# Optimization experiments

Measured on AMD Instinct MI355X. Metric: run time of the kernel, lower is better.

The kernel has to match this reference:

```python
import jax, jax.numpy as jnp
import numpy as np

B, S, D, E, H = 4, 2048, 1024, 8, 2048


def setup_inputs() -> dict:
    key = jax.random.key(0)
    ks = jax.random.split(key, 8)
    s_in = 1.0 / np.sqrt(D)   # torch Linear default init scale (uniform bound)
    s_hid = 1.0 / np.sqrt(H)
    return {
        "x": jax.random.normal(ks[0], (B, S, D), dtype=jnp.float32),
        "W1": jax.random.uniform(ks[1], (E, D, H), minval=-s_in, maxval=s_in, dtype=jnp.float32),
        "b1": jax.random.uniform(ks[2], (E, H), minval=-s_in, maxval=s_in, dtype=jnp.float32),
        "W2": jax.random.uniform(ks[3], (E, H, D), minval=-s_hid, maxval=s_hid, dtype=jnp.float32),
        "b2": jax.random.uniform(ks[4], (E, D), minval=-s_hid, maxval=s_hid, dtype=jnp.float32),
        "Wg": jax.random.uniform(ks[5], (D, E), minval=-s_in, maxval=s_in, dtype=jnp.float32),
        "bg": jax.random.uniform(ks[6], (E,), minval=-s_in, maxval=s_in, dtype=jnp.float32),
    }


def reference(x, W1, b1, W2, b2, Wg, bg):
    # All-experts dense MoE (eval mode: dropout is identity).
    # hidden: [B,S,E,H]
    h = jax.nn.relu(jnp.einsum("bsd,edh->bseh", x, W1) + b1)
    # expert outputs: [B,S,E,D]
    expert_out = jnp.einsum("bseh,ehd->bsed", h, W2) + b2
    # gate (raw linear, no softmax in original): [B,S,E]
    gate = jnp.einsum("bsd,de->bse", x, Wg) + bg
    # gate-weighted sum over experts -> [B,S,D]
    return jnp.einsum("bse,bsed->bsd", gate, expert_out)
```

## Files before the change

### kernel.cpp

```cpp
#include <hip/hip_runtime.h>

#define NTOK 8192
#define DDIM 1024
#define HDIM 2048
#define NEXP 8
#define GEXP 2

typedef unsigned short u16;
typedef short bf16x8 __attribute__((ext_vector_type(8)));
typedef float f32x4 __attribute__((ext_vector_type(4)));
typedef float float4_t __attribute__((ext_vector_type(4)));

__device__ __forceinline__ u16 f2bf(float f) {
  unsigned u = __float_as_uint(f);
  u += 0x7FFFu + ((u >> 16) & 1u);
  return (u16)(u >> 16);
}

#define GLOAD_LDS16(gp, lp)                                                     \
  __builtin_amdgcn_global_load_lds(                                             \
      (const __attribute__((address_space(1))) unsigned int*)(gp),              \
      (__attribute__((address_space(3))) unsigned int*)(lp), 16, 0, 0)

__global__ void k_prep(const float* __restrict__ x, const float* __restrict__ Wg,
                       const float* __restrict__ bg,
                       u16* __restrict__ xb, float* __restrict__ gate) {
  const int tok = (blockIdx.x * 256 + threadIdx.x) >> 6;
  const int lane = threadIdx.x & 63;
  const float* xr = x + (size_t)tok * DDIM;
  u16* xo = xb + (size_t)tok * DDIM;
  float s[NEXP];
#pragma unroll
  for (int e = 0; e < NEXP; ++e) s[e] = 0.f;
#pragma unroll
  for (int it = 0; it < 2; ++it) {
    const int d0 = lane * 8 + it * 512;
    float4_t v0 = *(const float4_t*)(xr + d0);
    float4_t v1 = *(const float4_t*)(xr + d0 + 4);
    union { bf16x8 v; u16 h[8]; } u;
    u.h[0] = f2bf(v0.x); u.h[1] = f2bf(v0.y); u.h[2] = f2bf(v0.z); u.h[3] = f2bf(v0.w);
    u.h[4] = f2bf(v1.x); u.h[5] = f2bf(v1.y); u.h[6] = f2bf(v1.z); u.h[7] = f2bf(v1.w);
    *(bf16x8*)(xo + d0) = u.v;
    float xv[8] = {v0.x, v0.y, v0.z, v0.w, v1.x, v1.y, v1.z, v1.w};
#pragma unroll
    for (int j = 0; j < 8; ++j) {
      const float4_t w0 = *(const float4_t*)(Wg + (size_t)(d0 + j) * NEXP);
      const float4_t w1 = *(const float4_t*)(Wg + (size_t)(d0 + j) * NEXP + 4);
      s[0] += xv[j] * w0.x; s[1] += xv[j] * w0.y;
      s[2] += xv[j] * w0.z; s[3] += xv[j] * w0.w;
      s[4] += xv[j] * w1.x; s[5] += xv[j] * w1.y;
      s[6] += xv[j] * w1.z; s[7] += xv[j] * w1.w;
    }
  }
#pragma unroll
  for (int off = 32; off; off >>= 1)
#pragma unroll
    for (int e = 0; e < NEXP; ++e) s[e] += __shfl_down(s[e], off);
  if (lane == 0) {
#pragma unroll
    for (int e = 0; e < NEXP; ++e) gate[(size_t)tok * NEXP + e] = s[e] + bg[e];
  }
}

__global__ void k_transpose(const float* __restrict__ in, u16* __restrict__ out,
                            int R, int C, size_t oexp, int orstride) {
  __shared__ float t[64][65];
  const int rb = blockIdx.x * 64, cb = blockIdx.y * 64;
  const float* pin = in + (size_t)blockIdx.z * R * C;
  u16* pout = out + (size_t)blockIdx.z * oexp;
  const int tid = threadIdx.x;
  {
    const int r = tid >> 4;
    const int c4 = (tid & 15) * 4;
#pragma unroll
    for (int i = 0; i < 4; ++i) {
      float4_t v = *(const float4_t*)(pin + (size_t)(rb + r + 16 * i) * C + cb + c4);
      t[r + 16 * i][c4 + 0] = v.x;
      t[r + 16 * i][c4 + 1] = v.y;
      t[r + 16 * i][c4 + 2] = v.z;
      t[r + 16 * i][c4 + 3] = v.w;
    }
  }
  __syncthreads();
  {
    const int oc = tid >> 3;
    const int r8 = (tid & 7) * 8;
#pragma unroll
    for (int jp = 0; jp < 2; ++jp) {
      const int ocol = oc + 32 * jp;
      union { bf16x8 v; u16 h[8]; } u;
#pragma unroll
      for (int k = 0; k < 8; ++k) u.h[k] = f2bf(t[r8 + k][ocol]);
      *(bf16x8*)(pout + (size_t)(cb + ocol) * orstride + rb + r8) = u.v;
    }
  }
}

template <int TM, int TN, int MODE, int BCH>
__global__ __launch_bounds__(512, 2) void k_gemm(
    const u16* __restrict__ A, int lda,
    const u16* __restrict__ Bt, int ldb,
    const float* __restrict__ bias,
    const float* __restrict__ gate, int ebase,
    void* __restrict__ Cout, int ldc,
    int K, int accum, int ca, int cb, int cgcols) {
  constexpr int WN = TN / 64;
  constexpr int BUFE = (TM + TN) * 64;
  __shared__ __align__(16) u16 lds[3 * BUFE];
  const int tid = threadIdx.x, lane = tid & 63, wid = tid >> 6;
  const int wm = wid / WN, wn = wid % WN;

  const int wg = blockIdx.x;
  const int xcd = wg & 7, lo = wg >> 3;
  const int cr = xcd / cgcols, cc = xcd % cgcols;
  const int tm = cr * ca + lo / cb;
  const int tn = cc * cb + lo % cb;
  const int bm = tm * TM, bn = tn * TN;

  const int srow = tid >> 3;
  const int scol = ((tid & 7) ^ (srow & 7)) << 3;
  const u16* gA = A + (size_t)(bm + srow) * lda + scol;
  const u16* gB = Bt + (size_t)(bn + srow) * ldb + scol;
  const int dofs = wid * 512;

  u16* buf0 = lds;
  u16* buf1 = lds + BUFE;
  u16* buf2 = lds + 2 * BUFE;

#define BOFF(kt) (BCH ? ((size_t)((kt) >> 5) * ((size_t)DDIM * HDIM) +          \
                         (size_t)((kt) & 31) * 64)                              \
                      : (size_t)(kt) * 64)
#define STAGE(dst, kt)                                                          \
  { _Pragma("unroll") for (int c_ = 0; c_ < TM / 64; ++c_)                      \
      GLOAD_LDS16(gA + (size_t)(c_ * 64) * lda + (size_t)(kt) * 64,             \
                  (dst) + c_ * 4096 + dofs);                                    \
    _Pragma("unroll") for (int c_ = 0; c_ < TN / 64; ++c_)                      \
      GLOAD_LDS16(gB + (size_t)(c_ * 64) * ldb + BOFF(kt),                      \
                  (dst) + (TM / 64 + c_) * 4096 + dofs); }

  const int fr = lane & 15, fq = lane >> 4, xr = fr & 7;
  const int so0 = ((0 + fq) ^ xr) << 3;
  const int so1 = ((4 + fq) ^ xr) << 3;

  f32x4 acc[4][4] = {};
  const int nkt = K >> 6;

  STAGE(buf0, 0);
  STAGE(buf1, 1);
  u16 *bC = buf0, *bN = buf1, *bF = buf2;

#pragma unroll 1
  for (int t = 0; t < nkt; ++t) {
    if (t + 1 < nkt) { asm volatile("s_waitcnt vmcnt(6)" ::: "memory"); }
    else             { asm volatile("s_waitcnt vmcnt(0)" ::: "memory"); }
    __builtin_amdgcn_s_barrier();
    __builtin_amdgcn_sched_barrier(0);
    if (t + 2 < nkt) STAGE(bF, t + 2);
    const u16* aP = bC;
    const u16* bP = bC + TM * 64;
    bf16x8 av[4][2], bv[4][2];
#pragma unroll
    for (int mi = 0; mi < 4; ++mi) {
      const int rb_ = (wm * 64 + mi * 16 + fr) << 6;
      av[mi][0] = *(const bf16x8*)(aP + rb_ + so0);
      av[mi][1] = *(const bf16x8*)(aP + rb_ + so1);
    }
#pragma unroll
    for (int ni = 0; ni < 4; ++ni) {
      const int rb_ = (wn * 64 + ni * 16 + fr) << 6;
      bv[ni][0] = *(const bf16x8*)(bP + rb_ + so0);
      bv[ni][1] = *(const bf16x8*)(bP + rb_ + so1);
    }
    __builtin_amdgcn_s_setprio(1);
#pragma unroll
    for (int mi = 0; mi < 4; ++mi)
#pragma unroll
      for (int ni = 0; ni < 4; ++ni) {
        acc[mi][ni] = __builtin_amdgcn_mfma_f32_16x16x32_bf16(
            av[mi][0], bv[ni][0], acc[mi][ni], 0, 0, 0);
        acc[mi][ni] = __builtin_amdgcn_mfma_f32_16x16x32_bf16(
            av[mi][1], bv[ni][1], acc[mi][ni], 0, 0, 0);
      }
    __builtin_amdgcn_s_setprio(0);
    u16* tp = bC; bC = bN; bN = bF; bF = tp;
  }

  if (MODE == 1) {
    u16* O = (u16*)Cout;
    const int e = ebase + (bn >> 11);
    float bcol[4];
#pragma unroll
    for (int ni = 0; ni < 4; ++ni) bcol[ni] = bias[bn + wn * 64 + ni * 16 + fr];
#pragma unroll
    for (int mi = 0; mi < 4; ++mi) {
#pragma unroll
      for (int j = 0; j < 4; ++j) {
        const int r = bm + wm * 64 + mi * 16 + fq * 4 + j;
        const float g = gate[(size_t)r * NEXP + e];
#pragma unroll
        for (int ni = 0; ni < 4; ++ni) {
          float v = fmaxf(acc[mi][ni][j] + bcol[ni], 0.f) * g;
          O[(size_t)r * ldc + bn + wn * 64 + ni * 16 + fr] = f2bf(v);
        }
      }
    }
  } else {
    float* O = (float*)Cout;
    float b2c[4][NEXP];
    if (!accum) {
#pragma unroll
      for (int ni = 0; ni < 4; ++ni)
#pragma unroll
        for (int e = 0; e < NEXP; ++e)
          b2c[ni][e] = bias[(size_t)e * DDIM + bn + wn * 64 + ni * 16 + fr];
    }
#pragma unroll
    for (int mi = 0; mi < 4; ++mi) {
#pragma unroll
      for (int j = 0; j < 4; ++j) {
        const int r = bm + wm * 64 + mi * 16 + fq * 4 + j;
        if (!accum) {
          float g8[NEXP];
#pragma unroll
          for (int e = 0; e < NEXP; ++e) g8[e] = gate[(size_t)r * NEXP + e];
#pragma unroll
          for (int ni = 0; ni < 4; ++ni) {
            float v = acc[mi][ni][j];
#pragma unroll
            for (int e = 0; e < NEXP; ++e) v += g8[e] * b2c[ni][e];
            O[(size_t)r * DDIM + bn + wn * 64 + ni * 16 + fr] = v;
          }
        } else {
#pragma unroll
          for (int ni = 0; ni < 4; ++ni) {
            const size_t idx = (size_t)r * DDIM + bn + wn * 64 + ni * 16 + fr;
            O[idx] += acc[mi][ni][j];
          }
        }
      }
    }
  }
#undef STAGE
#undef BOFF
}

extern "C" void kernel_launch(void* const* d_in, const int* in_sizes, int n_in,
                              void* d_out, int out_size, void* d_ws, size_t ws_size,
                              hipStream_t stream) {
  (void)in_sizes; (void)n_in; (void)out_size;
  const float* x  = (const float*)d_in[0];
  const float* W1 = (const float*)d_in[1];
  const float* b1 = (const float*)d_in[2];
  const float* W2 = (const float*)d_in[3];
  const float* b2 = (const float*)d_in[4];
  const float* Wg = (const float*)d_in[5];
  const float* bg = (const float*)d_in[6];
  float* out = (float*)d_out;

  size_t o_xb   = 0;
  size_t o_w1t  = o_xb  + (size_t)NTOK * DDIM * 2;
  size_t o_w2t  = o_w1t + (size_t)NEXP * HDIM * DDIM * 2;
  size_t o_gate = o_w2t + (size_t)NEXP * DDIM * HDIM * 2;
  size_t o_h    = o_gate + (size_t)NTOK * NEXP * 4;
  size_t need   = o_h   + (size_t)NTOK * GEXP * HDIM * 2;
  if (ws_size < need) return;

  u16*   xb   = (u16*)((char*)d_ws + o_xb);
  u16*   W1t  = (u16*)((char*)d_ws + o_w1t);
  u16*   W2t  = (u16*)((char*)d_ws + o_w2t);
  float* gate = (float*)((char*)d_ws + o_gate);
  u16*   hbuf = (u16*)((char*)d_ws + o_h);

  k_prep<<<NTOK / 4, 256, 0, stream>>>(x, Wg, bg, xb, gate);
  dim3 g1(DDIM / 64, HDIM / 64, NEXP);
  k_transpose<<<g1, 256, 0, stream>>>(W1, W1t, DDIM, HDIM, (size_t)HDIM * DDIM, DDIM);
  dim3 g2(HDIM / 64, DDIM / 64, NEXP);
  k_transpose<<<g2, 256, 0, stream>>>(W2, W2t, HDIM, DDIM, (size_t)DDIM * HDIM, HDIM);

  const int Ng = GEXP * HDIM;
  for (int g = 0; g < NEXP / GEXP; ++g) {
    k_gemm<256, 128, 1, 0><<<1024, 512, 0, stream>>>(
        xb, DDIM, W1t + (size_t)g * Ng * DDIM, DDIM,
        b1 + (size_t)g * Ng, gate, g * GEXP,
        hbuf, Ng, DDIM, 0, 16, 8, 4);
    k_gemm<128, 256, 2, 1><<<256, 512, 0, stream>>>(
        hbuf, Ng, W2t + (size_t)g * GEXP * DDIM * HDIM, HDIM,
        b2, gate, 0,
        out, DDIM, Ng, g > 0, 8, 4, 1);
  }
}
```

Measured before the change: 683.7 us.

## Load A fragments directly from global into registers, stage only B via LDS

Measured after the change: 1.356 ms. 1.98x slower.

```diff
diff --git a/kernel.cpp b/kernel.cpp
--- a/kernel.cpp
+++ b/kernel.cpp
@@ -96,7 +96,7 @@
   }
 }
 
-template <int TM, int TN, int MODE, int BCH>
+template <int NWM, int NWN, int MODE, int BCH>
 __global__ __launch_bounds__(512, 2) void k_gemm(
     const u16* __restrict__ A, int lda,
     const u16* __restrict__ Bt, int ldb,
@@ -104,11 +104,13 @@
     const float* __restrict__ gate, int ebase,
     void* __restrict__ Cout, int ldc,
     int K, int accum, int ca, int cb, int cgcols) {
-  constexpr int WN = TN / 64;
-  constexpr int BUFE = (TM + TN) * 64;
+  constexpr int TM = NWM * 64;
+  constexpr int TN = NWN * 64;
+  constexpr int NB = TN / 64;
+  constexpr int BUFE = TN * 64;
   __shared__ __align__(16) u16 lds[3 * BUFE];
   const int tid = threadIdx.x, lane = tid & 63, wid = tid >> 6;
-  const int wm = wid / WN, wn = wid % WN;
+  const int wm = wid / NWN, wn = wid % NWN;
 
   const int wg = blockIdx.x;
   const int xcd = wg & 7, lo = wg >> 3;
@@ -119,70 +121,75 @@
 
   const int srow = tid >> 3;
   const int scol = ((tid & 7) ^ (srow & 7)) << 3;
-  const u16* gA = A + (size_t)(bm + srow) * lda + scol;
   const u16* gB = Bt + (size_t)(bn + srow) * ldb + scol;
   const int dofs = wid * 512;
 
-  u16* buf0 = lds;
-  u16* buf1 = lds + BUFE;
-  u16* buf2 = lds + 2 * BUFE;
+  const int fr = lane & 15, fq = lane >> 4, xr = fr & 7;
+  const u16* gAa = A + (size_t)(bm + wm * 64 + fr) * lda + fq * 8;
+
+  u16* b0 = lds;
+  u16* b1 = lds + BUFE;
+  u16* b2 = lds + 2 * BUFE;
 
 #define BOFF(kt) (BCH ? ((size_t)((kt) >> 5) * ((size_t)DDIM * HDIM) +          \
                          (size_t)((kt) & 31) * 64)                              \
                       : (size_t)(kt) * 64)
-#define STAGE(dst, kt)                                                          \
-  { _Pragma("unroll") for (int c_ = 0; c_ < TM / 64; ++c_)                      \
-      GLOAD_LDS16(gA + (size_t)(c_ * 64) * lda + (size_t)(kt) * 64,             \
-                  (dst) + c_ * 4096 + dofs);                                    \
-    _Pragma("unroll") for (int c_ = 0; c_ < TN / 64; ++c_)                      \
+#define STAGE_B(dst, kt)                                                        \
+  { _Pragma("unroll") for (int c_ = 0; c_ < NB; ++c_)                           \
       GLOAD_LDS16(gB + (size_t)(c_ * 64) * ldb + BOFF(kt),                      \
-                  (dst) + (TM / 64 + c_) * 4096 + dofs); }
-
-  const int fr = lane & 15, fq = lane >> 4, xr = fr & 7;
+                  (dst) + c_ * 4096 + dofs); }
+#define LOAD_A(dst, kt)                                                         \
+  { _Pragma("unroll") for (int mi_ = 0; mi_ < 4; ++mi_)                         \
+    _Pragma("unroll") for (int kk_ = 0; kk_ < 2; ++kk_)                         \
+      (dst)[mi_ * 2 + kk_] = *(const bf16x8*)(gAa +                             \
+          (size_t)(mi_ * 16) * lda + (size_t)(kt) * 64 + kk_ * 32); }
+#define VMW_NB()                                                                \
+  { if (NB == 2) asm volatile("s_waitcnt vmcnt(2)" ::: "memory");               \
+    else         asm volatile("s_waitcnt vmcnt(4)" ::: "memory"); }
+
   const int so0 = ((0 + fq) ^ xr) << 3;
   const int so1 = ((4 + fq) ^ xr) << 3;
 
   f32x4 acc[4][4] = {};
   const int nkt = K >> 6;
 
-  STAGE(buf0, 0);
-  STAGE(buf1, 1);
-  u16 *bC = buf0, *bN = buf1, *bF = buf2;
+  bf16x8 aA[8], aB[8];
+
+  STAGE_B(b0, 0);
+  LOAD_A(aA, 0);
+  STAGE_B(b1, 1);
+  u16 *bC = b0, *bN = b1, *bF = b2;
+
+#define TILE_BODY(t, aU, aL)                                                    \
+  {                                                                             \
+    if ((t) == nkt - 1) { asm volatile("s_waitcnt vmcnt(0)" ::: "memory"); }    \
+    else                { VMW_NB(); }                                           \
+    __builtin_amdgcn_s_barrier();                                               \
+    __builtin_amdgcn_sched_barrier(0);                                          \
+    if ((t) + 1 < nkt) LOAD_A(aL, (t) + 1);                                     \
+    if ((t) + 2 < nkt) STAGE_B(bF, (t) + 2);                                    \
+    bf16x8 bv[4][2];                                                            \
+    _Pragma("unroll") for (int ni_ = 0; ni_ < 4; ++ni_) {                       \
+      const int rb_ = (wn * 64 + ni_ * 16 + fr) << 6;                           \
+      bv[ni_][0] = *(const bf16x8*)(bC + rb_ + so0);                            \
+      bv[ni_][1] = *(const bf16x8*)(bC + rb_ + so1);                            \
+    }                                                                           \
+    __builtin_amdgcn_s_setprio(1);                                              \
+    _Pragma("unroll") for (int mi_ = 0; mi_ < 4; ++mi_)                         \
+    _Pragma("unroll") for (int ni_ = 0; ni_ < 4; ++ni_) {                       \
+      acc[mi_][ni_] = __builtin_amdgcn_mfma_f32_16x16x32_bf16(                  \
+          (aU)[mi_ * 2 + 0], bv[ni_][0], acc[mi_][ni_], 0, 0, 0);               \
+      acc[mi_][ni_] = __builtin_amdgcn_mfma_f32_16x16x32_bf16(                  \
+          (aU)[mi_ * 2 + 1], bv[ni_][1], acc[mi_][ni_], 0, 0, 0);               \
+    }                                                                           \
+    __builtin_amdgcn_s_setprio(0);                                              \
+    u16* tp_ = bC; bC = bN; bN = bF; bF = tp_;                                  \
+  }
 
 #pragma unroll 1
-  for (int t = 0; t < nkt; ++t) {
-    if (t + 1 < nkt) { asm volatile("s_waitcnt vmcnt(6)" ::: "memory"); }
-    else             { asm volatile("s_waitcnt vmcnt(0)" ::: "memory"); }
-    __builtin_amdgcn_s_barrier();
-    __builtin_amdgcn_sched_barrier(0);
-    if (t + 2 < nkt) STAGE(bF, t + 2);
-    const u16* aP = bC;
-    const u16* bP = bC + TM * 64;
-    bf16x8 av[4][2], bv[4][2];
-#pragma unroll
-    for (int mi = 0; mi < 4; ++mi) {
-      const int rb_ = (wm * 64 + mi * 16 + fr) << 6;
-      av[mi][0] = *(const bf16x8*)(aP + rb_ + so0);
-      av[mi][1] = *(const bf16x8*)(aP + rb_ + so1);
-    }
-#pragma unroll
-    for (int ni = 0; ni < 4; ++ni) {
-      const int rb_ = (wn * 64 + ni * 16 + fr) << 6;
-      bv[ni][0] = *(const bf16x8*)(bP + rb_ + so0);
-      bv[ni][1] = *(const bf16x8*)(bP + rb_ + so1);
-    }
-    __builtin_amdgcn_s_setprio(1);
-#pragma unroll
-    for (int mi = 0; mi < 4; ++mi)
-#pragma unroll
-      for (int ni = 0; ni < 4; ++ni) {
-        acc[mi][ni] = __builtin_amdgcn_mfma_f32_16x16x32_bf16(
-            av[mi][0], bv[ni][0], acc[mi][ni], 0, 0, 0);
-        acc[mi][ni] = __builtin_amdgcn_mfma_f32_16x16x32_bf16(
-            av[mi][1], bv[ni][1], acc[mi][ni], 0, 0, 0);
-      }
-    __builtin_amdgcn_s_setprio(0);
-    u16* tp = bC; bC = bN; bN = bF; bF = tp;
+  for (int tp = 0; tp < nkt; tp += 2) {
+    TILE_BODY(tp, aA, aB);
+    TILE_BODY(tp + 1, aB, aA);
   }
 
   if (MODE == 1) {
@@ -240,7 +247,10 @@
       }
     }
   }
-#undef STAGE
+#undef TILE_BODY
+#undef STAGE_B
+#undef LOAD_A
+#undef VMW_NB
 #undef BOFF
 }
 
@@ -279,11 +289,11 @@
 
   const int Ng = GEXP * HDIM;
   for (int g = 0; g < NEXP / GEXP; ++g) {
-    k_gemm<256, 128, 1, 0><<<1024, 512, 0, stream>>>(
+    k_gemm<4, 2, 1, 0><<<1024, 512, 0, stream>>>(
         xb, DDIM, W1t + (size_t)g * Ng * DDIM, DDIM,
         b1 + (size_t)g * Ng, gate, g * GEXP,
         hbuf, Ng, DDIM, 0, 16, 8, 4);
-    k_gemm<128, 256, 2, 1><<<256, 512, 0, stream>>>(
+    k_gemm<2, 4, 2, 1><<<256, 512, 0, stream>>>(
         hbuf, Ng, W2t + (size_t)g * GEXP * DDIM * HDIM, HDIM,
         b2, gate, 0,
         out, DDIM, Ng, g > 0, 8, 4, 1);
```

## Replace GEMM with lagged half-tile MFMA pipeline and group four experts per pass

Applied to the files above, without the earlier changes.

Result: faster. 626.6 us (-8.3%).

```diff
diff --git a/kernel.cpp b/kernel.cpp
--- a/kernel.cpp
+++ b/kernel.cpp
@@ -4,7 +4,6 @@
 #define DDIM 1024
 #define HDIM 2048
 #define NEXP 8
-#define GEXP 2
 
 typedef unsigned short u16;
 typedef short bf16x8 __attribute__((ext_vector_type(8)));
@@ -21,6 +20,10 @@
   __builtin_amdgcn_global_load_lds(                                             \
       (const __attribute__((address_space(1))) unsigned int*)(gp),              \
       (__attribute__((address_space(3))) unsigned int*)(lp), 16, 0, 0)
+
+#define VMW(n) asm volatile("s_waitcnt vmcnt(" #n ")" ::: "memory")
+#define ENTRYB()                                                                \
+  { __builtin_amdgcn_s_barrier(); __builtin_amdgcn_sched_barrier(0); }
 
 __global__ void k_prep(const float* __restrict__ x, const float* __restrict__ Wg,
                        const float* __restrict__ bg,
@@ -96,26 +99,23 @@
   }
 }
 
-template <int TM, int TN, int MODE, int BCH>
-__global__ __launch_bounds__(512, 2) void k_gemm(
+template <int MODE, int BCH>
+__global__ __launch_bounds__(512, 2) void k_lag(
     const u16* __restrict__ A, int lda,
     const u16* __restrict__ Bt, int ldb,
     const float* __restrict__ bias,
     const float* __restrict__ gate, int ebase,
     void* __restrict__ Cout, int ldc,
-    int K, int accum, int ca, int cb, int cgcols) {
-  constexpr int WN = TN / 64;
-  constexpr int BUFE = (TM + TN) * 64;
-  __shared__ __align__(16) u16 lds[3 * BUFE];
+    int accum, int nk, int ca, int cb, int cgcols) {
+  __shared__ __align__(16) u16 lds[49152];
   const int tid = threadIdx.x, lane = tid & 63, wid = tid >> 6;
-  const int wm = wid / WN, wn = wid % WN;
-
+  const int wm = wid >> 2, wn = wid & 3;
   const int wg = blockIdx.x;
   const int xcd = wg & 7, lo = wg >> 3;
   const int cr = xcd / cgcols, cc = xcd % cgcols;
   const int tm = cr * ca + lo / cb;
   const int tn = cc * cb + lo % cb;
-  const int bm = tm * TM, bn = tn * TN;
+  const int bm = tm * 128, bn = tn * 256;
 
   const int srow = tid >> 3;
   const int scol = ((tid & 7) ^ (srow & 7)) << 3;
@@ -123,125 +123,142 @@
   const u16* gB = Bt + (size_t)(bn + srow) * ldb + scol;
   const int dofs = wid * 512;
 
-  u16* buf0 = lds;
-  u16* buf1 = lds + BUFE;
-  u16* buf2 = lds + 2 * BUFE;
-
-#define BOFF(kt) (BCH ? ((size_t)((kt) >> 5) * ((size_t)DDIM * HDIM) +          \
-                         (size_t)((kt) & 31) * 64)                              \
-                      : (size_t)(kt) * 64)
-#define STAGE(dst, kt)                                                          \
-  { _Pragma("unroll") for (int c_ = 0; c_ < TM / 64; ++c_)                      \
-      GLOAD_LDS16(gA + (size_t)(c_ * 64) * lda + (size_t)(kt) * 64,             \
-                  (dst) + c_ * 4096 + dofs);                                    \
-    _Pragma("unroll") for (int c_ = 0; c_ < TN / 64; ++c_)                      \
-      GLOAD_LDS16(gB + (size_t)(c_ * 64) * ldb + BOFF(kt),                      \
-                  (dst) + (TM / 64 + c_) * 4096 + dofs); }
+  u16* aB0 = lds;          u16* bB0 = lds + 8192;
+  u16* aB1 = lds + 24576;  u16* bB1 = lds + 32768;
 
   const int fr = lane & 15, fq = lane >> 4, xr = fr & 7;
   const int so0 = ((0 + fq) ^ xr) << 3;
   const int so1 = ((4 + fq) ^ xr) << 3;
 
-  f32x4 acc[4][4] = {};
-  const int nkt = K >> 6;
-
-  STAGE(buf0, 0);
-  STAGE(buf1, 1);
-  u16 *bC = buf0, *bN = buf1, *bF = buf2;
+  f32x4 acc[2][4][2] = {};
+  bf16x8 avA[8], avB[8], bv0[2][2], bv1[2][2];
+
+#define BOFF(ts) (BCH ? ((size_t)((ts) >> 5) * ((size_t)DDIM * HDIM) +          \
+                         (size_t)((ts) & 31) * 64)                              \
+                      : (size_t)(ts) * 64)
+#define L_SA(dst, ts)                                                           \
+  { GLOAD_LDS16(gA + (size_t)(ts) * 64, (dst) + dofs);                          \
+    GLOAD_LDS16(gA + (size_t)64 * lda + (size_t)(ts) * 64,                      \
+                (dst) + 4096 + dofs); }
+#define L_SB(dst, hh, ts)                                                       \
+  { GLOAD_LDS16(gB + (size_t)((hh)*128     ) * ldb + BOFF(ts),                  \
+                (dst) + ((hh)*128     ) * 64 + dofs);                           \
+    GLOAD_LDS16(gB + (size_t)((hh)*128 + 64) * ldb + BOFF(ts),                  \
+                (dst) + ((hh)*128 + 64) * 64 + dofs); }
+#define L_RDA(DST, src)                                                         \
+  { _Pragma("unroll") for (int i_ = 0; i_ < 4; ++i_) {                          \
+      const int rb_ = (wm * 64 + i_ * 16 + fr) << 6;                            \
+      (DST)[i_ * 2 + 0] = *(const bf16x8*)((src) + rb_ + so0);                  \
+      (DST)[i_ * 2 + 1] = *(const bf16x8*)((src) + rb_ + so1); } }
+#define L_RDB(DST, src, NH)                                                     \
+  { _Pragma("unroll") for (int n_ = 0; n_ < 2; ++n_) {                          \
+      const int rb_ = ((NH)*128 + wn * 32 + n_ * 16 + fr) << 6;                 \
+      (DST)[n_][0] = *(const bf16x8*)((src) + rb_ + so0);                       \
+      (DST)[n_][1] = *(const bf16x8*)((src) + rb_ + so1); } }
+#define L_MMA(Q, AV, BV)                                                        \
+  { __builtin_amdgcn_s_setprio(1);                                              \
+    _Pragma("unroll") for (int k_ = 0; k_ < 2; ++k_)                            \
+    _Pragma("unroll") for (int i_ = 0; i_ < 4; ++i_)                            \
+    _Pragma("unroll") for (int n_ = 0; n_ < 2; ++n_)                            \
+      acc[Q][i_][n_] = __builtin_amdgcn_mfma_f32_16x16x32_bf16(                 \
+          (AV)[i_ * 2 + k_], (BV)[n_][k_], acc[Q][i_][n_], 0, 0, 0);            \
+    __builtin_amdgcn_s_setprio(0); }
+
+#define L_ITER(T, AV, AVP, aCur, bCur, aNx, bNx)                                \
+  {                                                                             \
+    VMW(2); ENTRYB();                                                           \
+    L_RDA(AV, aCur);                                                            \
+    L_RDB(bv0, bCur, 0);                                                        \
+    if ((T) + 1 < nk) { L_SA(aNx, (T) + 1); L_SB(bNx, 0, (T) + 1); }            \
+    if ((T) > 0) L_MMA(1, AVP, bv1);                                            \
+    if ((T) + 1 < nk) { VMW(4); } else { VMW(0); }                              \
+    ENTRYB();                                                                   \
+    L_RDB(bv1, bCur, 1);                                                        \
+    if ((T) + 1 < nk) L_SB(bNx, 1, (T) + 1);                                    \
+    L_MMA(0, AV, bv0);                                                          \
+  }
+
+  L_SA(aB0, 0); L_SB(bB0, 0, 0); L_SB(bB0, 1, 0);
 
 #pragma unroll 1
-  for (int t = 0; t < nkt; ++t) {
-    if (t + 1 < nkt) { asm volatile("s_waitcnt vmcnt(6)" ::: "memory"); }
-    else             { asm volatile("s_waitcnt vmcnt(0)" ::: "memory"); }
-    __builtin_amdgcn_s_barrier();
-    __builtin_amdgcn_sched_barrier(0);
-    if (t + 2 < nkt) STAGE(bF, t + 2);
-    const u16* aP = bC;
-    const u16* bP = bC + TM * 64;
-    bf16x8 av[4][2], bv[4][2];
-#pragma unroll
-    for (int mi = 0; mi < 4; ++mi) {
-      const int rb_ = (wm * 64 + mi * 16 + fr) << 6;
-      av[mi][0] = *(const bf16x8*)(aP + rb_ + so0);
-      av[mi][1] = *(const bf16x8*)(aP + rb_ + so1);
-    }
-#pragma unroll
-    for (int ni = 0; ni < 4; ++ni) {
-      const int rb_ = (wn * 64 + ni * 16 + fr) << 6;
-      bv[ni][0] = *(const bf16x8*)(bP + rb_ + so0);
-      bv[ni][1] = *(const bf16x8*)(bP + rb_ + so1);
-    }
-    __builtin_amdgcn_s_setprio(1);
-#pragma unroll
-    for (int mi = 0; mi < 4; ++mi)
-#pragma unroll
-      for (int ni = 0; ni < 4; ++ni) {
-        acc[mi][ni] = __builtin_amdgcn_mfma_f32_16x16x32_bf16(
-            av[mi][0], bv[ni][0], acc[mi][ni], 0, 0, 0);
-        acc[mi][ni] = __builtin_amdgcn_mfma_f32_16x16x32_bf16(
-            av[mi][1], bv[ni][1], acc[mi][ni], 0, 0, 0);
-      }
-    __builtin_amdgcn_s_setprio(0);
-    u16* tp = bC; bC = bN; bN = bF; bF = tp;
-  }
+  for (int tt = 0; tt < nk; tt += 2) {
+    L_ITER(tt,     avA, avB, aB0, bB0, aB1, bB1);
+    L_ITER(tt + 1, avB, avA, aB1, bB1, aB0, bB0);
+  }
+  L_MMA(1, avB, bv1);
 
   if (MODE == 1) {
     u16* O = (u16*)Cout;
-    const int e = ebase + (bn >> 11);
-    float bcol[4];
-#pragma unroll
-    for (int ni = 0; ni < 4; ++ni) bcol[ni] = bias[bn + wn * 64 + ni * 16 + fr];
-#pragma unroll
-    for (int mi = 0; mi < 4; ++mi) {
-#pragma unroll
-      for (int j = 0; j < 4; ++j) {
-        const int r = bm + wm * 64 + mi * 16 + fq * 4 + j;
-        const float g = gate[(size_t)r * NEXP + e];
-#pragma unroll
-        for (int ni = 0; ni < 4; ++ni) {
-          float v = fmaxf(acc[mi][ni][j] + bcol[ni], 0.f) * g;
-          O[(size_t)r * ldc + bn + wn * 64 + ni * 16 + fr] = f2bf(v);
-        }
-      }
-    }
-  } else {
-    float* O = (float*)Cout;
-    float b2c[4][NEXP];
-    if (!accum) {
-#pragma unroll
-      for (int ni = 0; ni < 4; ++ni)
-#pragma unroll
-        for (int e = 0; e < NEXP; ++e)
-          b2c[ni][e] = bias[(size_t)e * DDIM + bn + wn * 64 + ni * 16 + fr];
-    }
-#pragma unroll
-    for (int mi = 0; mi < 4; ++mi) {
-#pragma unroll
-      for (int j = 0; j < 4; ++j) {
-        const int r = bm + wm * 64 + mi * 16 + fq * 4 + j;
-        if (!accum) {
-          float g8[NEXP];
-#pragma unroll
-          for (int e = 0; e < NEXP; ++e) g8[e] = gate[(size_t)r * NEXP + e];
-#pragma unroll
-          for (int ni = 0; ni < 4; ++ni) {
-            float v = acc[mi][ni][j];
-#pragma unroll
-            for (int e = 0; e < NEXP; ++e) v += g8[e] * b2c[ni][e];
-            O[(size_t)r * DDIM + bn + wn * 64 + ni * 16 + fr] = v;
-          }
-        } else {
-#pragma unroll
-          for (int ni = 0; ni < 4; ++ni) {
-            const size_t idx = (size_t)r * DDIM + bn + wn * 64 + ni * 16 + fr;
-            O[idx] += acc[mi][ni][j];
+#pragma unroll
+    for (int NH = 0; NH < 2; ++NH) {
+      const int cb0 = bn + NH * 128 + wn * 32;
+      const int e = ebase + (cb0 >> 11);
+      float bcol[2];
+#pragma unroll
+      for (int n = 0; n < 2; ++n) bcol[n] = bias[cb0 + n * 16 + fr];
+#pragma unroll
+      for (int i = 0; i < 4; ++i) {
+#pragma unroll
+        for (int j = 0; j < 4; ++j) {
+          const int r = bm + wm * 64 + i * 16 + fq * 4 + j;
+          const float g = gate[(size_t)r * NEXP + e];
+#pragma unroll
+          for (int n = 0; n < 2; ++n) {
+            float v = fmaxf(acc[NH][i][n][j] + bcol[n], 0.f) * g;
+            O[(size_t)r * ldc + cb0 + n * 16 + fr] = f2bf(v);
           }
         }
       }
     }
-  }
-#undef STAGE
+  } else {
+    float* O = (float*)Cout;
+    float b2c[2][2][NEXP];
+    if (!accum) {
+#pragma unroll
+      for (int nh = 0; nh < 2; ++nh)
+#pragma unroll
+        for (int n = 0; n < 2; ++n)
+#pragma unroll
+          for (int e = 0; e < NEXP; ++e)
+            b2c[nh][n][e] = bias[(size_t)e * DDIM + bn + nh * 128 + wn * 32 + n * 16 + fr];
+    }
+#pragma unroll
+    for (int NH = 0; NH < 2; ++NH) {
+      const int cb0 = bn + NH * 128 + wn * 32;
+#pragma unroll
+      for (int i = 0; i < 4; ++i) {
+#pragma unroll
+        for (int j = 0; j < 4; ++j) {
+          const int r = bm + wm * 64 + i * 16 + fq * 4 + j;
+          if (!accum) {
+            float g8[NEXP];
+#pragma unroll
+            for (int e = 0; e < NEXP; ++e) g8[e] = gate[(size_t)r * NEXP + e];
+#pragma unroll
+            for (int n = 0; n < 2; ++n) {
+              float v = acc[NH][i][n][j];
+#pragma unroll
+              for (int e = 0; e < NEXP; ++e) v += g8[e] * b2c[NH][n][e];
+              O[(size_t)r * DDIM + cb0 + n * 16 + fr] = v;
+            }
+          } else {
+#pragma unroll
+            for (int n = 0; n < 2; ++n) {
+              const size_t idx = (size_t)r * DDIM + cb0 + n * 16 + fr;
+              O[idx] += acc[NH][i][n][j];
+            }
+          }
+        }
+      }
+    }
+  }
 #undef BOFF
+#undef L_SA
+#undef L_SB
+#undef L_RDA
+#undef L_RDB
+#undef L_MMA
+#undef L_ITER
 }
 
 extern "C" void kernel_launch(void* const* d_in, const int* in_sizes, int n_in,
@@ -262,8 +279,10 @@
   size_t o_w2t  = o_w1t + (size_t)NEXP * HDIM * DDIM * 2;
   size_t o_gate = o_w2t + (size_t)NEXP * DDIM * HDIM * 2;
   size_t o_h    = o_gate + (size_t)NTOK * NEXP * 4;
-  size_t need   = o_h   + (size_t)NTOK * GEXP * HDIM * 2;
-  if (ws_size < need) return;
+
+  int G = 4;
+  if (o_h + (size_t)NTOK * G * HDIM * 2 > ws_size) G = 2;
+  if (o_h + (size_t)NTOK * G * HDIM * 2 > ws_size) return;
 
   u16*   xb   = (u16*)((char*)d_ws + o_xb);
   u16*   W1t  = (u16*)((char*)d_ws + o_w1t);
@@ -277,15 +296,17 @@
   dim3 g2(HDIM / 64, DDIM / 64, NEXP);
   k_transpose<<<g2, 256, 0, stream>>>(W2, W2t, HDIM, DDIM, (size_t)DDIM * HDIM, HDIM);
 
-  const int Ng = GEXP * HDIM;
-  for (int g = 0; g < NEXP / GEXP; ++g) {
-    k_gemm<256, 128, 1, 0><<<1024, 512, 0, stream>>>(
-        xb, DDIM, W1t + (size_t)g * Ng * DDIM, DDIM,
-        b1 + (size_t)g * Ng, gate, g * GEXP,
-        hbuf, Ng, DDIM, 0, 16, 8, 4);
-    k_gemm<128, 256, 2, 1><<<256, 512, 0, stream>>>(
-        hbuf, Ng, W2t + (size_t)g * GEXP * DDIM * HDIM, HDIM,
+  const int KW = G * HDIM;
+  const int ca1 = (G == 4) ? 32 : 16;
+  const int cg1 = (G == 4) ? 4 : 2;
+  for (int g = 0; g < NEXP / G; ++g) {
+    k_lag<1, 0><<<(NTOK / 128) * (KW / 256), 512, 0, stream>>>(
+        xb, DDIM, W1t + (size_t)g * KW * DDIM, DDIM,
+        b1 + (size_t)g * KW, gate, g * G,
+        hbuf, KW, 0, DDIM / 64, ca1, 8, cg1);
+    k_lag<2, 1><<<256, 512, 0, stream>>>(
+        hbuf, KW, W2t + (size_t)g * G * DDIM * HDIM, HDIM,
         b2, gate, 0,
-        out, DDIM, Ng, g > 0, 8, 4, 1);
-  }
-}
+        out, DDIM, g > 0, KW / 64, 8, 4, 1);
+  }
+}
```
